# Performance work log

Measured on AMD Instinct MI355X. Metric: run time of the kernel, lower is better.

Reference implementation:

```python
import jax, jax.numpy as jnp
import numpy as np

N = 2097152  # batch
D = 2        # DoF
H1 = 6       # hidden
EPS = 1e-3


def setup_inputs() -> dict:
    key = jax.random.key(0)
    ks = jax.random.split(key, 9)
    f32 = jnp.float32
    return {
        "x": jax.random.normal(ks[0], (N, 3 * D), dtype=f32),
        "W1": jax.random.normal(ks[1], (H1, D), dtype=f32) * 0.5,
        "b1": jax.random.normal(ks[2], (H1,), dtype=f32) * 0.1,
        "W2": jax.random.normal(ks[3], (D, H1), dtype=f32) * 0.5,
        "b2": jax.random.normal(ks[4], (D,), dtype=f32) * 0.1,
        "W3": jax.random.normal(ks[5], (D, H1), dtype=f32) * 0.5,
        "b3": jax.random.normal(ks[6], (D,), dtype=f32) * 0.1,
        "W4": jax.random.normal(ks[7], (1, H1), dtype=f32) * 0.5,
        "b4": jax.random.normal(ks[8], (1,), dtype=f32) * 0.1,
    }


def reference(x, W1, b1, W2, b2, W3, b3, W4, b4):
    n = x.shape[0]
    d = D
    dt = x.dtype
    q, q_dot, q_ddot = x[:, :d], x[:, d:2 * d], x[:, 2 * d:3 * d]

    h1 = jax.nn.relu(q @ W1.T + b1)          # [n,6]
    g = h1 @ W2.T + b2                        # [n,2]
    ld = jax.nn.relu(h1 @ W3.T + b3)          # [n,2] diagonal of L
    lo = h1 @ W4.T + b4                       # [n,1] strict-lower entry of L

    # analytic Jacobians through the ReLU MLP (relu masks are constants)
    dh1_dq = (h1 > 0).astype(dt)[:, :, None] * W1[None]      # [n,6,2]
    dld_dh1 = (ld > 0).astype(dt)[:, :, None] * W3[None]     # [n,2,6]
    dld_dq = dld_dh1 @ dh1_dq                                 # [n,2,2]
    dlo_dq = jnp.matmul(W4, dh1_dq)[:, 0, :]                  # [n,2]

    dld_dqi = jnp.swapaxes(dld_dq, 1, 2)                      # [n,d,d]: [b,i,j]=d ld_j / d q_i
    dld_dt = jnp.einsum('nij,nj->ni', dld_dq, q_dot)          # [n,d]
    dlo_dt = jnp.einsum('nj,nj->n', dlo_dq, q_dot)            # [n]

    ar = jnp.arange(d)
    # assemble lower-triangular L and its time / positional derivatives (d=2)
    L = jnp.zeros((n, d, d), dt).at[:, 1, 0].set(lo[:, 0]).at[:, ar, ar].set(ld)
    dL_dt = jnp.zeros((n, d, d), dt).at[:, 1, 0].set(dlo_dt).at[:, ar, ar].set(dld_dt)
    dL_dqi = jnp.zeros((n, d, d, d), dt).at[:, :, 1, 0].set(dlo_dq).at[:, :, ar, ar].set(dld_dqi)

    LT = jnp.swapaxes(L, 1, 2)
    H = LT @ L + EPS * jnp.eye(d, dtype=dt)                   # [n,d,d]
    dH_dt = L @ jnp.swapaxes(dL_dt, 1, 2) + dL_dt @ LT        # [n,d,d]

    # quadratic Coriolis term: q_dot^T (dL_dqi L^T + L dL_dqi^T) q_dot per i
    A = dL_dqi @ LT[:, None] + L[:, None] @ jnp.swapaxes(dL_dqi, -1, -2)  # [n,d,d,d]
    quad = jnp.einsum('nj,nijk,nk->ni', q_dot, A, q_dot)      # [n,d]

    tau = (jnp.einsum('nij,nj->ni', H, q_ddot)
           + jnp.einsum('nij,nj->ni', dH_dt, q_dot)
           + quad + g)
    return tau
```

## Files before the change

kernel.cpp:

```cpp
#include <hip/hip_runtime.h>

#define NROWS 2097152
#define EPSV 0.001f

__global__ __launch_bounds__(256) void delan_tau_kernel(
    const float* __restrict__ x,
    const float* __restrict__ W1, const float* __restrict__ b1,
    const float* __restrict__ W2, const float* __restrict__ b2,
    const float* __restrict__ W3, const float* __restrict__ b3,
    const float* __restrict__ W4, const float* __restrict__ b4,
    float* __restrict__ out)
{
    const int t = blockIdx.x * blockDim.x + threadIdx.x;

    const float4* x4 = reinterpret_cast<const float4*>(x) + 6u * (unsigned)t;
    const float4 v0 = x4[0];
    const float4 v1 = x4[1];
    const float4 v2 = x4[2];
    const float4 v3 = x4[3];
    const float4 v4 = x4[4];
    const float4 v5 = x4[5];

    float w1[12], bb1[6], w2[12], bb2[2], w3[12], bb3[2], w4[6];
    #pragma unroll
    for (int i = 0; i < 12; ++i) w1[i] = W1[i];
    #pragma unroll
    for (int i = 0; i < 6; ++i)  bb1[i] = b1[i];
    #pragma unroll
    for (int i = 0; i < 12; ++i) w2[i] = W2[i];
    bb2[0] = b2[0]; bb2[1] = b2[1];
    #pragma unroll
    for (int i = 0; i < 12; ++i) w3[i] = W3[i];
    bb3[0] = b3[0]; bb3[1] = b3[1];
    #pragma unroll
    for (int i = 0; i < 6; ++i)  w4[i] = W4[i];
    const float bb4 = b4[0];

    const float rows[4][6] = {
        { v0.x, v0.y, v0.z, v0.w, v1.x, v1.y },
        { v1.z, v1.w, v2.x, v2.y, v2.z, v2.w },
        { v3.x, v3.y, v3.z, v3.w, v4.x, v4.y },
        { v4.z, v4.w, v5.x, v5.y, v5.z, v5.w }
    };

    float res[8];

    #pragma unroll
    for (int rr = 0; rr < 4; ++rr) {
        const float q0 = rows[rr][0], q1 = rows[rr][1];
        const float qd0 = rows[rr][2], qd1 = rows[rr][3];
        const float qdd0 = rows[rr][4], qdd1 = rows[rr][5];

        float h[6], m[6];
        #pragma unroll
        for (int j = 0; j < 6; ++j) {
            const float pre = fmaf(w1[2 * j], q0, fmaf(w1[2 * j + 1], q1, bb1[j]));
            const bool pos = pre > 0.0f;
            h[j] = pos ? pre : 0.0f;
            m[j] = pos ? 1.0f : 0.0f;
        }

        float g0 = bb2[0], g1 = bb2[1], ldp0 = bb3[0], ldp1 = bb3[1], lo = bb4;
        #pragma unroll
        for (int j = 0; j < 6; ++j) {
            g0   = fmaf(h[j], w2[j],     g0);
            g1   = fmaf(h[j], w2[6 + j], g1);
            ldp0 = fmaf(h[j], w3[j],     ldp0);
            ldp1 = fmaf(h[j], w3[6 + j], ldp1);
            lo   = fmaf(h[j], w4[j],     lo);
        }
        const float p = ldp0 > 0.0f ? ldp0 : 0.0f;
        const float s = ldp1 > 0.0f ? ldp1 : 0.0f;
        const float md0 = ldp0 > 0.0f ? 1.0f : 0.0f;
        const float md1 = ldp1 > 0.0f ? 1.0f : 0.0f;
        const float r = lo;

        float s00 = 0.f, s01 = 0.f, s10 = 0.f, s11 = 0.f, c0 = 0.f, c1 = 0.f;
        #pragma unroll
        for (int j = 0; j < 6; ++j) {
            const float d0 = m[j] * w1[2 * j];
            const float d1 = m[j] * w1[2 * j + 1];
            s00 = fmaf(w3[j],     d0, s00);
            s01 = fmaf(w3[j],     d1, s01);
            s10 = fmaf(w3[6 + j], d0, s10);
            s11 = fmaf(w3[6 + j], d1, s11);
            c0  = fmaf(w4[j],     d0, c0);
            c1  = fmaf(w4[j],     d1, c1);
        }
        const float dq00 = md0 * s00, dq01 = md0 * s01;
        const float dq10 = md1 * s10, dq11 = md1 * s11;

        const float a = fmaf(dq00, qd0, dq01 * qd1);
        const float b = fmaf(dq10, qd0, dq11 * qd1);
        const float c = fmaf(c0,   qd0, c1   * qd1);

        const float H00 = fmaf(p, p, fmaf(r, r, EPSV));
        const float H01 = r * s;
        const float H11 = fmaf(s, s, EPSV);

        const float dH00 = 2.0f * a * p;
        const float dH01 = fmaf(p, c, a * r);
        const float dH11 = 2.0f * fmaf(r, c, s * b);

        const float k00 = qd0 * qd0, k01 = qd0 * qd1, k11 = qd1 * qd1;
        const float quad0 = 2.0f * (dq00 * p * k00 + fmaf(p, c0, dq00 * r) * k01
                                    + fmaf(r, c0, s * dq10) * k11);
        const float quad1 = 2.0f * (dq01 * p * k00 + fmaf(p, c1, dq01 * r) * k01
                                    + fmaf(r, c1, s * dq11) * k11);

        const float tau0 = fmaf(H00, qdd0, fmaf(H01, qdd1,
                           fmaf(dH00, qd0, fmaf(dH01, qd1, quad0 + g0))));
        const float tau1 = fmaf(H01, qdd0, fmaf(H11, qdd1,
                           fmaf(dH01, qd0, fmaf(dH11, qd1, quad1 + g1))));
        res[2 * rr + 0] = tau0;
        res[2 * rr + 1] = tau1;
    }

    float4* o4 = reinterpret_cast<float4*>(out) + 2u * (unsigned)t;
    o4[0] = make_float4(res[0], res[1], res[2], res[3]);
    o4[1] = make_float4(res[4], res[5], res[6], res[7]);
}

extern "C" void kernel_launch(void* const* d_in, const int* in_sizes, int n_in,
                              void* d_out, int out_size, void* d_ws, size_t ws_size,
                              hipStream_t stream) {
    const float* x  = (const float*)d_in[0];
    const float* W1 = (const float*)d_in[1];
    const float* b1 = (const float*)d_in[2];
    const float* W2 = (const float*)d_in[3];
    const float* b2 = (const float*)d_in[4];
    const float* W3 = (const float*)d_in[5];
    const float* b3 = (const float*)d_in[6];
    const float* W4 = (const float*)d_in[7];
    const float* b4 = (const float*)d_in[8];
    float* out = (float*)d_out;

    const int threads = 256;
    const int nthreads_total = NROWS / 4;
    const int blocks = nthreads_total / threads;
    delan_tau_kernel<<<blocks, threads, 0, stream>>>(x, W1, b1, W2, b2, W3, b3,
                                                     W4, b4, out);
}
```

Measured before the change: 104.7 us.

## Stage input through shared memory for coalesced loads and halve rows per thread

Each block now loads its input tile with fully coalesced float4 reads into LDS, synchronises, then each thread reads its own contiguous three float4s from LDS. Rows per thread drop from four to two and the grid doubles, so the output store becomes one coalesced float4 per thread. This targets the poor coalescing of the old 96-byte-strided per-thread loads. In exchange it adds a barrier, LDS traffic with possible bank conflicts, and twice as many threads doing the weight loads.

```diff
diff --git a/kernel.cpp b/kernel.cpp
--- a/kernel.cpp
+++ b/kernel.cpp
@@ -11,15 +11,14 @@
     const float* __restrict__ W4, const float* __restrict__ b4,
     float* __restrict__ out)
 {
-    const int t = blockIdx.x * blockDim.x + threadIdx.x;
+    __shared__ float4 xs[768];
+    const int tid = threadIdx.x;
+    const unsigned base = (unsigned)blockIdx.x * 768u;
 
-    const float4* x4 = reinterpret_cast<const float4*>(x) + 6u * (unsigned)t;
-    const float4 v0 = x4[0];
-    const float4 v1 = x4[1];
-    const float4 v2 = x4[2];
-    const float4 v3 = x4[3];
-    const float4 v4 = x4[4];
-    const float4 v5 = x4[5];
+    const float4* x4 = reinterpret_cast<const float4*>(x);
+    const float4 a0 = x4[base + (unsigned)tid];
+    const float4 a1 = x4[base + 256u + (unsigned)tid];
+    const float4 a2 = x4[base + 512u + (unsigned)tid];
 
     float w1[12], bb1[6], w2[12], bb2[2], w3[12], bb3[2], w4[6];
     #pragma unroll
@@ -36,17 +35,23 @@
     for (int i = 0; i < 6; ++i)  w4[i] = W4[i];
     const float bb4 = b4[0];
 
-    const float rows[4][6] = {
+    xs[tid]        = a0;
+    xs[256 + tid]  = a1;
+    xs[512 + tid]  = a2;
+    __syncthreads();
+    const float4 v0 = xs[3 * tid + 0];
+    const float4 v1 = xs[3 * tid + 1];
+    const float4 v2 = xs[3 * tid + 2];
+
+    const float rows[2][6] = {
         { v0.x, v0.y, v0.z, v0.w, v1.x, v1.y },
-        { v1.z, v1.w, v2.x, v2.y, v2.z, v2.w },
-        { v3.x, v3.y, v3.z, v3.w, v4.x, v4.y },
-        { v4.z, v4.w, v5.x, v5.y, v5.z, v5.w }
+        { v1.z, v1.w, v2.x, v2.y, v2.z, v2.w }
     };
 
-    float res[8];
+    float res[4];
 
     #pragma unroll
-    for (int rr = 0; rr < 4; ++rr) {
+    for (int rr = 0; rr < 2; ++rr) {
         const float q0 = rows[rr][0], q1 = rows[rr][1];
         const float qd0 = rows[rr][2], qd1 = rows[rr][3];
         const float qdd0 = rows[rr][4], qdd1 = rows[rr][5];
@@ -116,9 +121,8 @@
         res[2 * rr + 1] = tau1;
     }
 
-    float4* o4 = reinterpret_cast<float4*>(out) + 2u * (unsigned)t;
-    o4[0] = make_float4(res[0], res[1], res[2], res[3]);
-    o4[1] = make_float4(res[4], res[5], res[6], res[7]);
+    reinterpret_cast<float4*>(out)[(unsigned)blockIdx.x * 256u + (unsigned)tid] =
+        make_float4(res[0], res[1], res[2], res[3]);
 }
 
 extern "C" void kernel_launch(void* const* d_in, const int* in_sizes, int n_in,
@@ -136,7 +140,7 @@
     float* out = (float*)d_out;
 
     const int threads = 256;
-    const int nthreads_total = NROWS / 4;
+    const int nthreads_total = NROWS / 2;
     const int blocks = nthreads_total / threads;
     delan_tau_kernel<<<blocks, threads, 0, stream>>>(x, W1, b1, W2, b2, W3, b3,
                                                      W4, b4, out);
```

Result: faster. 101.6 us (-3.0%).
